# Optimization experiments

Hardware: AMD Instinct MI355X
Metric: run time of the kernel (lower is better)

Reference implementation:

```python
import jax, jax.numpy as jnp
import numpy as np

N = 50000       # nodes
E = 800000      # edges (avg degree 16)
IN = 256        # in_features
HEAD = 4        # attention heads (conv1/conv2 out_channels)
F_OUT = 32      # mlp output features per head


def setup_inputs() -> dict:
    key = jax.random.key(0)
    ks = jax.random.split(key, 6)
    feat = jax.random.normal(ks[0], (N, IN), dtype=jnp.float32)
    edge_index = jax.random.randint(ks[1], (2, E), 0, N, dtype=jnp.int64)
    s = 1.0 / np.sqrt(IN)
    # mlp: Linear(IN -> HEAD*F_OUT)
    W_mlp = jax.random.uniform(ks[2], (IN, HEAD * F_OUT), jnp.float32, -s, s)
    b_mlp = jnp.zeros((HEAD * F_OUT,), jnp.float32)
    # conv1/conv2: 1x1 Conv1d(IN -> HEAD) == linear projection
    W1 = jax.random.uniform(ks[3], (HEAD, IN), jnp.float32, -s, s)
    b1 = jnp.zeros((HEAD,), jnp.float32)
    W2 = jax.random.uniform(ks[4], (HEAD, IN), jnp.float32, -s, s)
    b2 = jnp.zeros((HEAD,), jnp.float32)
    eps = jnp.zeros((1,), jnp.float32)  # trainable eps, init 0
    return {"feat": feat, "edge_index": edge_index, "W_mlp": W_mlp,
            "b_mlp": b_mlp, "W1": W1, "b1": b1, "W2": W2, "b2": b2,
            "eps": eps}


def reference(feat, edge_index, W_mlp, b_mlp, W1, b1, W2, b2, eps):
    n = feat.shape[0]
    head = W1.shape[0]
    # mlp: [N, IN] -> [N, head*F] -> [head, N, F]
    x = (feat @ W_mlp + b_mlp).reshape(n, head, -1).transpose(1, 0, 2)
    # 1x1 conv projections -> per-node attention logits [head, N]
    h1 = (feat @ W1.T + b1).T
    h2 = (feat @ W2.T + b2).T
    src = edge_index[0]  # edge[0]
    dst = edge_index[1]  # edge[1]
    # per-edge attention value, relu (dropout=0 -> identity): [head, E]
    v = jax.nn.relu(h1[:, src] + h2[:, dst])
    # gather neighbor features and weight: [head, E, F]
    msg = x[:, dst, :] * v[:, :, None]
    # scatter-add into destination nodes indexed by src: [N, head, F]
    agg = jax.ops.segment_sum(msg.transpose(1, 0, 2), src, num_segments=n)
    h_prime = agg.transpose(1, 0, 2) + eps[0] * x   # [head, N, F]
    # permute(1,0,2).reshape(N, -1) -> [N, head*F]
    return h_prime.transpose(1, 0, 2).reshape(n, -1)
```

## Files before the change

### kernel.cpp

```cpp
#include <hip/hip_runtime.h>

#define NN   50000
#define EE   800000
#define INF  256
#define COUT 128
#define BTROWS 144
#define PROJ_BLOCKS 782
#define CAP  52

#define NB   196
#define BCAP 4608
#define EPB  4096
#define SC_BLOCKS ((EE + EPB - 1) / EPB)
#define BT_BLOCKS 144

typedef __attribute__((ext_vector_type(8))) short short8;
typedef __attribute__((ext_vector_type(4))) float f32x4;

__device__ __forceinline__ float b2f(unsigned short u) {
    union { unsigned int i; float f; } c;
    c.i = ((unsigned int)u) << 16;
    return c.f;
}
__device__ __forceinline__ unsigned short f2b(float f) {
    union { float f; unsigned int i; } c;
    c.f = f;
    unsigned int i = c.i;
    unsigned int lsb = (i >> 16) & 1u;
    i += 0x7fffu + lsb;
    return (unsigned short)(i >> 16);
}
__device__ __forceinline__ float blo(unsigned int u) {
    union { unsigned int i; float f; } c; c.i = u << 16; return c.f;
}
__device__ __forceinline__ float bhi(unsigned int u) {
    union { unsigned int i; float f; } c; c.i = u & 0xffff0000u; return c.f;
}

__global__ __launch_bounds__(256) void bt_scatter_kernel(
    const float* __restrict__ Wm, const float* __restrict__ W1,
    const float* __restrict__ W2,
    unsigned short* __restrict__ BT,
    const int* __restrict__ edge,
    int* __restrict__ bcnt,
    unsigned int* __restrict__ bedges)
{
    __shared__ int lhist[NB];
    __shared__ int lbase[NB];
    const int t = threadIdx.x;

    if (blockIdx.x < BT_BLOCKS) {
        const int n = blockIdx.x;
        const int k = t;
        float v;
        if      (n < 128) v = Wm[k * COUT + n];
        else if (n < 132) v = W1[(n - 128) * INF + k];
        else if (n < 136) v = W2[(n - 132) * INF + k];
        else              v = 0.f;
        BT[n * INF + k] = f2b(v);
        return;
    }

    if (t < NB) lhist[t] = 0;
    __syncthreads();

    const int e0 = (blockIdx.x - BT_BLOCKS) * EPB;
    int s[16], d[16], pos[16];
    #pragma unroll
    for (int k = 0; k < 16; k++) {
        const int e = e0 + k * 256 + t;
        if (e < EE) {
            s[k] = edge[e];
            d[k] = edge[EE + e];
            pos[k] = atomicAdd(&lhist[s[k] >> 8], 1);
        } else {
            pos[k] = -1;
        }
    }
    __syncthreads();
    if (t < NB) lbase[t] = atomicAdd(&bcnt[t * 16], lhist[t]);
    __syncthreads();
    #pragma unroll
    for (int k = 0; k < 16; k++) {
        if (pos[k] >= 0) {
            const int b = s[k] >> 8;
            const int p = lbase[b] + pos[k];
            if (p < BCAP)
                bedges[b * BCAP + p] =
                    ((unsigned int)(s[k] & 255) << 16) | (unsigned int)d[k];
        }
    }
}

#define LSTRIDE 72
#define SMEM_A_BYTES (64 * LSTRIDE * 2)
#define SMEM_BYTES   (SMEM_A_BYTES + BTROWS * LSTRIDE * 2)
__global__ __launch_bounds__(256) void proj_build_kernel(
    const float* __restrict__ feat,
    const unsigned short* __restrict__ BT,
    const float* __restrict__ bm,
    const float* __restrict__ b1,
    const float* __restrict__ b2,
    unsigned short* __restrict__ x_out,
    unsigned short* __restrict__ hh,
    const unsigned int* __restrict__ bedges,
    const int* __restrict__ bcnt,
    unsigned short* __restrict__ sdst,
    int* __restrict__ cursor)
{
    __shared__ alignas(16) char smem[SMEM_BYTES];
    const int t = threadIdx.x;

    if (blockIdx.x >= PROJ_BLOCKS) {
        unsigned short* ladj = (unsigned short*)smem;
        int* lcur = (int*)(smem + 26624);
        const int b = blockIdx.x - PROJ_BLOCKS;
        lcur[t] = 0;
        __syncthreads();

        const int cnt = min(bcnt[b * 16], BCAP);
        for (int i = t; i < cnt; i += 256) {
            const unsigned int pk = bedges[b * BCAP + i];
            const int n = (int)(pk >> 16);
            const int p = atomicAdd(&lcur[n], 1);
            if (p < CAP) ladj[n * CAP + p] = (unsigned short)(pk & 0xffffu);
        }
        __syncthreads();

        const int node0 = b << 8;
        const int nvalid = min(256, NN - node0);
        const int nu8 = nvalid * (CAP / 4);
        unsigned long long* gs = (unsigned long long*)(sdst + (size_t)node0 * CAP);
        const unsigned long long* ls = (const unsigned long long*)ladj;
        for (int i = t; i < nu8; i += 256) gs[i] = ls[i];
        if (t < nvalid) cursor[node0 + t] = min(lcur[t], CAP);
        return;
    }

    short* lA = (short*)smem;
    short* lB = (short*)(smem + SMEM_A_BYTES);

    const int lane  = t & 63;
    const int wave  = t >> 6;
    const int quad  = lane >> 4;
    const int col   = lane & 15;
    const int node0 = blockIdx.x * 64;

    const int arow = t >> 4;
    const int ac4  = t & 15;
    const int brow = t >> 3;
    const int bc8  = t & 7;

    f32x4 acc[9];
    #pragma unroll
    for (int i = 0; i < 9; i++) acc[i] = (f32x4){0.f, 0.f, 0.f, 0.f};

    float4 fr[4];
    uint4  brg[5];

    #pragma unroll
    for (int p = 0; p < 4; p++) {
        const int grow = node0 + p * 16 + arow;
        fr[p] = (grow < NN) ? *(const float4*)(feat + grow * INF + ac4 * 4)
                            : make_float4(0.f, 0.f, 0.f, 0.f);
    }
    #pragma unroll
    for (int p = 0; p < 5; p++) {
        if (p * 256 + t < (BTROWS * 64) / 8)
            brg[p] = *(const uint4*)(BT + (p * 32 + brow) * INF + bc8 * 8);
    }

    #pragma unroll
    for (int kc = 0; kc < 4; kc++) {
        #pragma unroll
        for (int p = 0; p < 4; p++) {
            short4 s;
            s.x = (short)f2b(fr[p].x); s.y = (short)f2b(fr[p].y);
            s.z = (short)f2b(fr[p].z); s.w = (short)f2b(fr[p].w);
            *(short4*)&lA[(p * 16 + arow) * LSTRIDE + ac4 * 4] = s;
        }
        #pragma unroll
        for (int p = 0; p < 5; p++) {
            if (p * 256 + t < (BTROWS * 64) / 8)
                *(uint4*)&lB[(p * 32 + brow) * LSTRIDE + bc8 * 8] = brg[p];
        }
        __syncthreads();

        if (kc < 3) {
            const int k0 = (kc + 1) * 64;
            #pragma unroll
            for (int p = 0; p < 4; p++) {
                const int grow = node0 + p * 16 + arow;
                fr[p] = (grow < NN)
                    ? *(const float4*)(feat + grow * INF + k0 + ac4 * 4)
                    : make_float4(0.f, 0.f, 0.f, 0.f);
            }
            #pragma unroll
            for (int p = 0; p < 5; p++) {
                if (p * 256 + t < (BTROWS * 64) / 8)
                    brg[p] = *(const uint4*)(BT + (p * 32 + brow) * INF + k0 + bc8 * 8);
            }
        }

        #pragma unroll
        for (int ks = 0; ks < 2; ks++) {
            short8 a = *(const short8*)&lA[(wave * 16 + col) * LSTRIDE + ks * 32 + quad * 8];
            #pragma unroll
            for (int nt = 0; nt < 9; nt++) {
                short8 b = *(const short8*)&lB[(nt * 16 + col) * LSTRIDE + ks * 32 + quad * 8];
                acc[nt] = __builtin_amdgcn_mfma_f32_16x16x32_bf16(a, b, acc[nt], 0, 0, 0);
            }
        }
        __syncthreads();
    }

    const int rbase = node0 + wave * 16 + quad * 4;
    #pragma unroll
    for (int nt = 0; nt < 8; nt++) {
        const float bias = bm[nt * 16 + col];
        #pragma unroll
        for (int r = 0; r < 4; r++) {
            const int row = rbase + r;
            if (row < NN) x_out[row * COUT + nt * 16 + col] = f2b(acc[nt][r] + bias);
        }
    }
    if (col < 8) {
        const float bias = (col < 4) ? b1[col] : b2[col - 4];
        #pragma unroll
        for (int r = 0; r < 4; r++) {
            const int row = rbase + r;
            if (row < NN) hh[row * 8 + col] = f2b(acc[8][r] + bias);
        }
    }
}

__global__ __launch_bounds__(256) void accum_kernel(
    const int* __restrict__ cursor,
    const unsigned short* __restrict__ sdst,
    const unsigned short* __restrict__ x,
    const unsigned short* __restrict__ hh,
    const float* __restrict__ eps,
    float* __restrict__ out)
{
    const int lane = threadIdx.x & 63;
    const int node = blockIdx.x * 4 + (threadIdx.x >> 6);
    if (node >= NN) return;

    const int sub = lane & 15;
    const int g   = lane >> 4;
    const int h   = sub >> 2;

    const int deg = min(cursor[node], CAP);

    ushort4 h1u = *(const ushort4*)(hh + node * 8);

    int dv = 0;
    unsigned int vv01 = 0, vv23 = 0;
    if (lane < deg) {
        dv = (int)sdst[node * CAP + lane];
        ushort4 h2u = *(const ushort4*)(hh + dv * 8 + 4);
        const float v0 = b2f(h1u.x) + b2f(h2u.x);
        const float v1 = b2f(h1u.y) + b2f(h2u.y);
        const float v2 = b2f(h1u.z) + b2f(h2u.z);
        const float v3 = b2f(h1u.w) + b2f(h2u.w);
        vv01 = (unsigned int)f2b(v0) | ((unsigned int)f2b(v1) << 16);
        vv23 = (unsigned int)f2b(v2) | ((unsigned int)f2b(v3) << 16);
    }

    float acc[8];
    #pragma unroll
    for (int r = 0; r < 8; r++) acc[r] = 0.f;

    for (int i0 = 0; i0 < deg; i0 += 8) {
        const int idx0 = i0 + g;
        const int idx1 = i0 + 4 + g;
        const int d0 = __shfl(dv, idx0);
        const int d1 = __shfl(dv, idx1);
        const unsigned int u01a = (unsigned int)__shfl((int)vv01, idx0);
        const unsigned int u23a = (unsigned int)__shfl((int)vv23, idx0);
        const unsigned int u01b = (unsigned int)__shfl((int)vv01, idx1);
        const unsigned int u23b = (unsigned int)__shfl((int)vv23, idx1);
        const unsigned int uha = (h & 2) ? u23a : u01a;
        const unsigned int uhb = (h & 2) ? u23b : u01b;
        const float v0 = (h & 1) ? bhi(uha) : blo(uha);
        const float v1 = (h & 1) ? bhi(uhb) : blo(uhb);
        const bool p0 = (idx0 < deg) && (v0 > 0.f);
        const bool p1 = (idx1 < deg) && (v1 > 0.f);
        uint4 a0, a1;
        if (p0) a0 = *(const uint4*)(x + d0 * COUT + sub * 8);
        if (p1) a1 = *(const uint4*)(x + d1 * COUT + sub * 8);
        if (p0) {
            acc[0] = fmaf(blo(a0.x), v0, acc[0]);
            acc[1] = fmaf(bhi(a0.x), v0, acc[1]);
            acc[2] = fmaf(blo(a0.y), v0, acc[2]);
            acc[3] = fmaf(bhi(a0.y), v0, acc[3]);
            acc[4] = fmaf(blo(a0.z), v0, acc[4]);
            acc[5] = fmaf(bhi(a0.z), v0, acc[5]);
            acc[6] = fmaf(blo(a0.w), v0, acc[6]);
            acc[7] = fmaf(bhi(a0.w), v0, acc[7]);
        }
        if (p1) {
            acc[0] = fmaf(blo(a1.x), v1, acc[0]);
            acc[1] = fmaf(bhi(a1.x), v1, acc[1]);
            acc[2] = fmaf(blo(a1.y), v1, acc[2]);
            acc[3] = fmaf(bhi(a1.y), v1, acc[3]);
            acc[4] = fmaf(blo(a1.z), v1, acc[4]);
            acc[5] = fmaf(bhi(a1.z), v1, acc[5]);
            acc[6] = fmaf(blo(a1.w), v1, acc[6]);
            acc[7] = fmaf(bhi(a1.w), v1, acc[7]);
        }
    }

    #pragma unroll
    for (int r = 0; r < 8; r++) {
        acc[r] += __shfl_xor(acc[r], 16);
        acc[r] += __shfl_xor(acc[r], 32);
    }

    if (lane < 16) {
        const float e = eps[0];
        const uint4 u0 = *(const uint4*)(x + node * COUT + sub * 8);
        unsigned int uu[4] = {u0.x, u0.y, u0.z, u0.w};
        #pragma unroll
        for (int q = 0; q < 4; q++) {
            acc[2 * q]     = fmaf(e, blo(uu[q]), acc[2 * q]);
            acc[2 * q + 1] = fmaf(e, bhi(uu[q]), acc[2 * q + 1]);
        }
        float* o = out + node * COUT + sub * 8;
        *(float4*)(o)     = make_float4(acc[0], acc[1], acc[2], acc[3]);
        *(float4*)(o + 4) = make_float4(acc[4], acc[5], acc[6], acc[7]);
    }
}

extern "C" void kernel_launch(void* const* d_in, const int* in_sizes, int n_in,
                              void* d_out, int out_size, void* d_ws, size_t ws_size,
                              hipStream_t stream) {
    const float* feat = (const float*)d_in[0];
    const int*   edge = (const int*)d_in[1];
    const float* Wm   = (const float*)d_in[2];
    const float* bm   = (const float*)d_in[3];
    const float* W1   = (const float*)d_in[4];
    const float* b1   = (const float*)d_in[5];
    const float* W2   = (const float*)d_in[6];
    const float* b2   = (const float*)d_in[7];
    const float* eps  = (const float*)d_in[8];

    char* ws = (char*)d_ws;
    unsigned short* x      = (unsigned short*)ws;
    unsigned short* hh     = (unsigned short*)(ws + 12800000);
    int*            cursor = (int*)(ws + 13600000);
    unsigned short* sdst   = (unsigned short*)(ws + 13800000);

    unsigned short* BT     = (unsigned short*)d_out;
    int*            bcnt   = (int*)((char*)d_out + 131072);
    unsigned int*   bedges = (unsigned int*)((char*)d_out + 262144);

    hipMemsetAsync(bcnt, 0, NB * 16 * sizeof(int), stream);
    bt_scatter_kernel<<<BT_BLOCKS + SC_BLOCKS, 256, 0, stream>>>(
        Wm, W1, W2, BT, edge, bcnt, bedges);
    proj_build_kernel<<<PROJ_BLOCKS + NB, 256, 0, stream>>>(
        feat, BT, bm, b1, b2, x, hh, bedges, bcnt, sdst, cursor);
    accum_kernel<<<(NN + 3) / 4, 256, 0, stream>>>(cursor, sdst, x, hh, eps,
                                                   (float*)d_out);
}
```

Baseline: 186.0 us.

## Drop register prefetch in projection GEMM and halve edges per scatter block

The projection GEMM loop no longer prefetches the next K-chunk of features and weights into registers while MFMAs run. Each chunk is now loaded and stored to LDS directly, the loop is no longer forced to unroll, and register pressure drops. The edge-bucketing kernel handles 2048 edges per block instead of 4096, which doubles the block count and reduces per-thread register arrays. The trade is more global atomics on the bucket counters and exposed load latency in the GEMM in exchange for possibly higher occupancy.

Result: faster. 171.2 us (-7.9%).

```diff
diff --git a/kernel.cpp b/kernel.cpp
--- a/kernel.cpp
+++ b/kernel.cpp
@@ -10,7 +10,7 @@
 
 #define NB   196
 #define BCAP 4608
-#define EPB  4096
+#define EPB  2048
 #define SC_BLOCKS ((EE + EPB - 1) / EPB)
 #define BT_BLOCKS 144
 
@@ -65,9 +65,9 @@
     __syncthreads();
 
     const int e0 = (blockIdx.x - BT_BLOCKS) * EPB;
-    int s[16], d[16], pos[16];
-    #pragma unroll
-    for (int k = 0; k < 16; k++) {
+    int s[8], d[8], pos[8];
+    #pragma unroll
+    for (int k = 0; k < 8; k++) {
         const int e = e0 + k * 256 + t;
         if (e < EE) {
             s[k] = edge[e];
@@ -81,7 +81,7 @@
     if (t < NB) lbase[t] = atomicAdd(&bcnt[t * 16], lhist[t]);
     __syncthreads();
     #pragma unroll
-    for (int k = 0; k < 16; k++) {
+    for (int k = 0; k < 8; k++) {
         if (pos[k] >= 0) {
             const int b = s[k] >> 8;
             const int p = lbase[b] + pos[k];
@@ -146,61 +146,36 @@
     const int col   = lane & 15;
     const int node0 = blockIdx.x * 64;
 
-    const int arow = t >> 4;
-    const int ac4  = t & 15;
-    const int brow = t >> 3;
-    const int bc8  = t & 7;
-
     f32x4 acc[9];
     #pragma unroll
     for (int i = 0; i < 9; i++) acc[i] = (f32x4){0.f, 0.f, 0.f, 0.f};
 
-    float4 fr[4];
-    uint4  brg[5];
-
-    #pragma unroll
-    for (int p = 0; p < 4; p++) {
-        const int grow = node0 + p * 16 + arow;
-        fr[p] = (grow < NN) ? *(const float4*)(feat + grow * INF + ac4 * 4)
-                            : make_float4(0.f, 0.f, 0.f, 0.f);
-    }
-    #pragma unroll
-    for (int p = 0; p < 5; p++) {
-        if (p * 256 + t < (BTROWS * 64) / 8)
-            brg[p] = *(const uint4*)(BT + (p * 32 + brow) * INF + bc8 * 8);
-    }
-
-    #pragma unroll
     for (int kc = 0; kc < 4; kc++) {
+        const int k0 = kc * 64;
         #pragma unroll
         for (int p = 0; p < 4; p++) {
+            const int idx = p * 256 + t;
+            const int row = idx >> 4;
+            const int c4  = idx & 15;
+            const int grow = node0 + row;
+            float4 f = make_float4(0.f, 0.f, 0.f, 0.f);
+            if (grow < NN) f = *(const float4*)(feat + grow * INF + k0 + c4 * 4);
             short4 s;
-            s.x = (short)f2b(fr[p].x); s.y = (short)f2b(fr[p].y);
-            s.z = (short)f2b(fr[p].z); s.w = (short)f2b(fr[p].w);
-            *(short4*)&lA[(p * 16 + arow) * LSTRIDE + ac4 * 4] = s;
+            s.x = (short)f2b(f.x); s.y = (short)f2b(f.y);
+            s.z = (short)f2b(f.z); s.w = (short)f2b(f.w);
+            *(short4*)&lA[row * LSTRIDE + c4 * 4] = s;
         }
         #pragma unroll
         for (int p = 0; p < 5; p++) {
-            if (p * 256 + t < (BTROWS * 64) / 8)
-                *(uint4*)&lB[(p * 32 + brow) * LSTRIDE + bc8 * 8] = brg[p];
+            const int idx = p * 256 + t;
+            if (idx < (BTROWS * 64) / 8) {
+                const int row = idx >> 3;
+                const int c8  = idx & 7;
+                uint4 u = *(const uint4*)(BT + row * INF + k0 + c8 * 8);
+                *(uint4*)&lB[row * LSTRIDE + c8 * 8] = u;
+            }
         }
         __syncthreads();
-
-        if (kc < 3) {
-            const int k0 = (kc + 1) * 64;
-            #pragma unroll
-            for (int p = 0; p < 4; p++) {
-                const int grow = node0 + p * 16 + arow;
-                fr[p] = (grow < NN)
-                    ? *(const float4*)(feat + grow * INF + k0 + ac4 * 4)
-                    : make_float4(0.f, 0.f, 0.f, 0.f);
-            }
-            #pragma unroll
-            for (int p = 0; p < 5; p++) {
-                if (p * 256 + t < (BTROWS * 64) / 8)
-                    brg[p] = *(const uint4*)(BT + (p * 32 + brow) * INF + k0 + bc8 * 8);
-            }
-        }
 
         #pragma unroll
         for (int ks = 0; ks < 2; ks++) {
```
